# Kernel tuning notes

Measured on AMD Instinct MI355X. Metric: run time of the kernel, lower is better.

The kernel has to match this reference:

```python
import jax, jax.numpy as jnp
import numpy as np

HIDDEN = 128
SIGMA_D = 0.2
SIGMA_A = 15.0
ANGLE_K = 8
FACTOR_A = 180.0 / (SIGMA_A * np.pi)


def pairwise_sqdist(x, y):
    # x: (B,N,3), y: (B,M,3) -> (B,N,M) squared distances, clamped at 0
    sq = (jnp.sum(x * x, -1)[:, :, None]
          + jnp.sum(y * y, -1)[:, None, :]
          - 2.0 * jnp.einsum('bnd,bmd->bnm', x, y))
    return jnp.maximum(sq, 0.0)


def sinusoidal_embedding(indices, d_model):
    # indices: (...,) -> (..., d_model) with interleaved sin/cos (GeoTransformer style)
    div_term = jnp.exp(jnp.arange(0, d_model, 2, dtype=indices.dtype)
                       * (-np.log(10000.0) / d_model))
    omegas = indices[..., None] * div_term  # (..., d_model/2)
    emb = jnp.stack([jnp.sin(omegas), jnp.cos(omegas)], axis=-1)
    return emb.reshape(*indices.shape, d_model)


def setup_inputs() -> dict:
    key = jax.random.key(0)
    k1, k2, k3, k4, k5 = jax.random.split(key, 5)
    B, N, H = 1, 512, HIDDEN
    bound = 1.0 / np.sqrt(H)
    return {
        'points': jax.random.normal(k1, (B, N, 3), dtype=jnp.float32),
        'Wd': jax.random.uniform(k2, (H, H), jnp.float32, -bound, bound),
        'bd': jax.random.uniform(k3, (H,), jnp.float32, -bound, bound),
        'Wa': jax.random.uniform(k4, (H, H), jnp.float32, -bound, bound),
        'ba': jax.random.uniform(k5, (H,), jnp.float32, -bound, bound),
    }


def _embedding_indices(points):
    # points: (B,N,3) -> d_indices (B,N,N), a_indices (B,N,N,k)
    B, N, _ = points.shape
    sqdist = pairwise_sqdist(points, points)
    dist_map = jnp.sqrt(sqdist)
    d_indices = dist_map / SIGMA_D
    # knn (exclude self = nearest)
    _, knn_idx = jax.lax.top_k(-dist_map, ANGLE_K + 1)  # (B,N,k+1)
    knn_idx = knn_idx[:, :, 1:]                         # (B,N,k)
    # gather neighbor coords: (B,N,k,3)
    knn_points = jax.vmap(lambda pts, idx: pts[idx])(points, knn_idx)
    ref = knn_points - points[:, :, None, :]            # (B,N,k,3)
    anc = points[:, None, :, :] - points[:, :, None, :]  # (B,N,N,3)
    ref_e = ref[:, :, None, :, :]                        # (B,N,1,k,3)
    anc_e = anc[:, :, :, None, :]                        # (B,N,N,1,3)
    cross = jnp.cross(ref_e, anc_e)                      # (B,N,N,k,3)
    sin_v = jnp.linalg.norm(cross, axis=-1)
    cos_v = jnp.sum(ref_e * anc_e, axis=-1)
    angles = jnp.arctan2(sin_v, cos_v)
    a_indices = angles * FACTOR_A
    return d_indices, a_indices


def reference(points, Wd, bd, Wa, ba):
    d_indices, a_indices = _embedding_indices(points)
    d_emb = sinusoidal_embedding(d_indices, HIDDEN)      # (B,N,N,H)
    d_emb = jnp.einsum('bnmh,gh->bnmg', d_emb, Wd) + bd
    a_emb = sinusoidal_embedding(a_indices, HIDDEN)      # (B,N,N,k,H)
    a_emb = jnp.einsum('bnmkh,gh->bnmkg', a_emb, Wa) + ba
    a_emb = jnp.max(a_emb, axis=3)                       # reduction_a == 'max'
    return d_emb + a_emb
```

## Files before the change

### kernel.cpp

```cpp
#include <hip/hip_runtime.h>
#include <math.h>

#define N_PTS 512
#define HID 128
#define KNN 8
#define MT 16
#define NTHREADS 256
#define NROWS 144

typedef __attribute__((ext_vector_type(8))) short short8_t;
typedef __attribute__((ext_vector_type(4))) float f32x4_t;

__device__ float g_refv[N_PTS * KNN * 3];
__device__ unsigned short g_wfrag[2 * 8 * 4 * 64 * 8];

__device__ __forceinline__ unsigned short f2bf(float f) {
    const unsigned int u = __float_as_uint(f);
    return (unsigned short)((u + 0x7FFFu + ((u >> 16) & 1u)) >> 16);
}

__global__ void __launch_bounds__(64) prep_kernel(
    const float* __restrict__ points, const float* __restrict__ Wd,
    const float* __restrict__ Wa)
{
    __shared__ float spts[N_PTS * 3];
    const int lane = threadIdx.x;
    const int n = blockIdx.x;

    for (int i = lane; i < N_PTS * 3; i += 64) spts[i] = points[i];
    __syncthreads();

    {
        const int idx = n * 64 + lane;
        const int sel = idx >> 14;
        const int rem = idx & 16383;
        const int gg = rem >> 7, kk = rem & 127;
        const int gtile = gg >> 4, glo = gg & 15;
        const int ktile = kk >> 5, kmid = (kk >> 3) & 3, j = kk & 7;
        const int fl = kmid * 16 + glo;
        const int dst = ((((sel * 8 + gtile) * 4 + ktile) * 64) + fl) * 8 + j;
        const float v = sel ? Wa[gg * HID + kk] : Wd[gg * HID + kk];
        g_wfrag[dst] = f2bf(v);
    }

    const float px = spts[n * 3 + 0], py = spts[n * 3 + 1], pz = spts[n * 3 + 2];
    unsigned long long keys[8];
#pragma unroll
    for (int j = 0; j < 8; ++j) {
        const int m = lane * 8 + j;
        const float dx = spts[m * 3 + 0] - px;
        const float dy = spts[m * 3 + 1] - py;
        const float dz = spts[m * 3 + 2] - pz;
        const float sq = dx * dx + dy * dy + dz * dz;
        keys[j] = ((unsigned long long)__float_as_uint(sq) << 32) | (unsigned)m;
    }
    for (int r = 0; r < 9; ++r) {
        unsigned long long lmin = ~0ULL;
#pragma unroll
        for (int j = 0; j < 8; ++j) lmin = keys[j] < lmin ? keys[j] : lmin;
        for (int s = 1; s < 64; s <<= 1) {
            const unsigned long long o = __shfl_xor(lmin, s, 64);
            lmin = o < lmin ? o : lmin;
        }
        const int mwin = (int)(unsigned)lmin;
        if ((mwin >> 3) == lane) keys[mwin & 7] = ~0ULL;
        if (r > 0 && lane == 0) {
            const int k = r - 1;
            g_refv[(n * KNN + k) * 3 + 0] = __fsub_rn(spts[mwin * 3 + 0], px);
            g_refv[(n * KNN + k) * 3 + 1] = __fsub_rn(spts[mwin * 3 + 1], py);
            g_refv[(n * KNN + k) * 3 + 2] = __fsub_rn(spts[mwin * 3 + 2], pz);
        }
    }
}

__global__ void __launch_bounds__(NTHREADS, 3) main_kernel(
    const float* __restrict__ points, const float* __restrict__ bd,
    const float* __restrict__ ba, float* __restrict__ out)
{
    __shared__ __align__(16) unsigned short sA[NROWS * HID];
    __shared__ __align__(16) float sBaseS[4][36];
    __shared__ float sRef[KNN][3];
    __shared__ float sPm[MT][3];
    __shared__ float sPn[3];

    const int t = threadIdx.x;
    const int n = blockIdx.y;
    const int m0 = blockIdx.x * MT;

    const int r0 = t >> 6;
    const int i  = t & 63;
    const float dv2 = expf(-0.14391156831212787f * (float)i) * 0.15915494309189535f;

    if (t < 3) sPn[t] = points[n * 3 + t];
    if (t >= 64 && t < 64 + MT * 3) { int q = t - 64;  sPm[q / 3][q % 3] = points[m0 * 3 + q]; }
    if (t >= 128 && t < 128 + KNN * 3) { int q = t - 128; sRef[q / 3][q % 3] = g_refv[n * KNN * 3 + q]; }
    __syncthreads();

    if (t < MT) {
        const float qx = sPm[t][0], qy = sPm[t][1], qz = sPm[t][2];
        const float sn = __fadd_rn(__fadd_rn(__fmul_rn(sPn[0], sPn[0]), __fmul_rn(sPn[1], sPn[1])), __fmul_rn(sPn[2], sPn[2]));
        const float sm = __fadd_rn(__fadd_rn(__fmul_rn(qx, qx), __fmul_rn(qy, qy)), __fmul_rn(qz, qz));
        float dot = __fmul_rn(sPn[0], qx);
        dot = fmaf(sPn[1], qy, dot);
        dot = fmaf(sPn[2], qz, dot);
        float sq = __fsub_rn(__fadd_rn(sn, sm), __fadd_rn(dot, dot));
        sq = fmaxf(sq, 0.0f);
        sBaseS[t & 3][t >> 2] = __fdiv_rn(__fsqrt_rn(sq), 0.2f);
    }
    if (t < MT * KNN) {
        const int pair = t >> 3, k = t & 7;
        const float ax = sPm[pair][0] - sPn[0];
        const float ay = sPm[pair][1] - sPn[1];
        const float az = sPm[pair][2] - sPn[2];
        const float rx = sRef[k][0], ry = sRef[k][1], rz = sRef[k][2];
        const float cx = ry * az - rz * ay;
        const float cy = rz * ax - rx * az;
        const float cz = rx * ay - ry * ax;
        const float sv = sqrtf(cx * cx + cy * cy + cz * cz);
        const float cv = rx * ax + ry * ay + rz * az;
        float ang;
        if (sv == 0.0f) ang = 0.0f;
        else            ang = atan2f(sv, cv);
        sBaseS[pair & 3][4 + 4 * k + (pair >> 2)] = ang * 3.8197186342054885f;
    }
    __syncthreads();

    {
        float rbase[36];
#pragma unroll
        for (int q = 0; q < 9; ++q) {
            const float4 v = *(const float4*)&sBaseS[r0][q * 4];
            rbase[q * 4 + 0] = v.x; rbase[q * 4 + 1] = v.y;
            rbase[q * 4 + 2] = v.z; rbase[q * 4 + 3] = v.w;
        }
        const unsigned base0 = (unsigned)((i * 4) ^ (r0 << 4)) + (unsigned)r0 * 256;
        char* const wr0 = (char*)sA + base0;
        char* const wr1 = (char*)sA + (base0 ^ 64u);
#pragma unroll
        for (int it = 0; it < 36; ++it) {
            const float rev0 = rbase[it] * dv2;
            const float rev  = rev0 - floorf(rev0);
            const float s = __builtin_amdgcn_sinf(rev);
            const float c = __builtin_amdgcn_cosf(rev);
            const unsigned int pack = __builtin_amdgcn_perm(
                __float_as_uint(c), __float_as_uint(s), 0x07060302u);
            char* const wp = (it & 1) ? wr1 : wr0;
            *(unsigned int*)(wp + it * 1024) = pack;
        }
    }
    __syncthreads();

    const int wid  = r0;
    const int lane = i;
    const int rlo  = lane & 15;
    const int kseg = lane >> 4;

    const short8_t* wf = (const short8_t*)g_wfrag;
    short8_t wdb[2][4], wab[2][4];
#pragma unroll
    for (int gt = 0; gt < 2; ++gt) {
        const int gtile = wid * 2 + gt;
#pragma unroll
        for (int kt = 0; kt < 4; ++kt) {
            wdb[gt][kt] = wf[(gtile * 4 + kt) * 64 + lane];
            wab[gt][kt] = wf[((8 + gtile) * 4 + kt) * 64 + lane];
        }
    }

    const char* sAb = (const char*)sA;
    f32x4_t accd[2] = {{0.f,0.f,0.f,0.f}, {0.f,0.f,0.f,0.f}};
#pragma unroll
    for (int kt = 0; kt < 4; ++kt) {
        int byte = rlo * 256 + kt * 64 + kseg * 16;
        byte ^= (rlo & 7) << 4;
        const short8_t af = *(const short8_t*)(sAb + byte);
        accd[0] = __builtin_amdgcn_mfma_f32_16x16x32_bf16(af, wdb[0][kt], accd[0], 0, 0, 0);
        accd[1] = __builtin_amdgcn_mfma_f32_16x16x32_bf16(af, wdb[1][kt], accd[1], 0, 0, 0);
    }

    f32x4_t amax[2] = {{0.f,0.f,0.f,0.f}, {0.f,0.f,0.f,0.f}};
#pragma unroll
    for (int k = 0; k < KNN; ++k) {
        f32x4_t acc0 = {0.f,0.f,0.f,0.f};
        f32x4_t acc1 = {0.f,0.f,0.f,0.f};
        const int rowb = MT + k * 16 + rlo;
#pragma unroll
        for (int kt = 0; kt < 4; ++kt) {
            int byte = rowb * 256 + kt * 64 + kseg * 16;
            byte ^= (rowb & 7) << 4;
            const short8_t af = *(const short8_t*)(sAb + byte);
            acc0 = __builtin_amdgcn_mfma_f32_16x16x32_bf16(af, wab[0][kt], acc0, 0, 0, 0);
            acc1 = __builtin_amdgcn_mfma_f32_16x16x32_bf16(af, wab[1][kt], acc1, 0, 0, 0);
        }
        if (k == 0) { amax[0] = acc0; amax[1] = acc1; }
        else {
#pragma unroll
            for (int r = 0; r < 4; ++r) {
                amax[0][r] = fmaxf(amax[0][r], acc0[r]);
                amax[1][r] = fmaxf(amax[1][r], acc1[r]);
            }
        }
    }

#pragma unroll
    for (int gt = 0; gt < 2; ++gt) {
        const int g = (wid * 2 + gt) * 16 + rlo;
        const float bdv = bd[g];
        const float bav = ba[g];
#pragma unroll
        for (int r = 0; r < 4; ++r) {
            const int m = m0 + kseg * 4 + r;
            out[(n * N_PTS + m) * HID + g] = accd[gt][r] + bdv + amax[gt][r] + bav;
        }
    }
}

extern "C" void kernel_launch(void* const* d_in, const int* in_sizes, int n_in,
                              void* d_out, int out_size, void* d_ws, size_t ws_size,
                              hipStream_t stream) {
    (void)in_sizes; (void)n_in; (void)out_size; (void)d_ws; (void)ws_size;
    const float* points = (const float*)d_in[0];
    const float* Wd     = (const float*)d_in[1];
    const float* bd     = (const float*)d_in[2];
    const float* Wa     = (const float*)d_in[3];
    const float* ba     = (const float*)d_in[4];
    float* out = (float*)d_out;

    prep_kernel<<<N_PTS, 64, 0, stream>>>(points, Wd, Wa);

    dim3 grid(N_PTS / MT, N_PTS);
    main_kernel<<<grid, NTHREADS, 0, stream>>>(points, bd, ba, out);
}
```

Baseline: 112.6 us.

## Process four m-tiles per block with double-buffered sinusoid fill overlapping MFMA

Each block now handles four 16-point m-tiles. The weight fragments are loaded once per block, and the A-operand LDS buffer is double-buffered. The sin/cos embedding for the next tile is computed and written while MFMAs run on the current tile, interleaved inside one unrolled loop. This amortizes the weight loads and block setup, and it hides transcendental ALU work behind matrix ops. The cost is a smaller grid, double the LDS use, and occupancy lowered from 3 to 2 blocks in the launch bounds.

Result: faster. 108.1 us (median of 2 runs) (-4.0%).

```diff
diff --git a/kernel.cpp b/kernel.cpp
--- a/kernel.cpp
+++ b/kernel.cpp
@@ -5,6 +5,7 @@
 #define HID 128
 #define KNN 8
 #define MT 16
+#define NTILES 4
 #define NTHREADS 256
 #define NROWS 144
 
@@ -73,30 +74,44 @@
     }
 }
 
-__global__ void __launch_bounds__(NTHREADS, 3) main_kernel(
+__global__ void __launch_bounds__(NTHREADS, 2) main_kernel(
     const float* __restrict__ points, const float* __restrict__ bd,
     const float* __restrict__ ba, float* __restrict__ out)
 {
-    __shared__ __align__(16) unsigned short sA[NROWS * HID];
-    __shared__ __align__(16) float sBaseS[4][36];
+    __shared__ __align__(16) unsigned short sA[2][NROWS * HID];
+    __shared__ __align__(16) float sBaseS[NTILES][4][36];
     __shared__ float sRef[KNN][3];
-    __shared__ float sPm[MT][3];
+    __shared__ float sPm[MT * NTILES][3];
     __shared__ float sPn[3];
 
     const int t = threadIdx.x;
     const int n = blockIdx.y;
-    const int m0 = blockIdx.x * MT;
+    const int M0 = blockIdx.x * (MT * NTILES);
 
     const int r0 = t >> 6;
     const int i  = t & 63;
     const float dv2 = expf(-0.14391156831212787f * (float)i) * 0.15915494309189535f;
 
+    const int wid = r0, lane = i;
+    const short8_t* wf = (const short8_t*)g_wfrag;
+    short8_t wdb[2][4], wab[2][4];
+#pragma unroll
+    for (int gt = 0; gt < 2; ++gt) {
+        const int gtile = wid * 2 + gt;
+#pragma unroll
+        for (int kt = 0; kt < 4; ++kt) {
+            wdb[gt][kt] = wf[(gtile * 4 + kt) * 64 + lane];
+            wab[gt][kt] = wf[((8 + gtile) * 4 + kt) * 64 + lane];
+        }
+    }
+
     if (t < 3) sPn[t] = points[n * 3 + t];
-    if (t >= 64 && t < 64 + MT * 3) { int q = t - 64;  sPm[q / 3][q % 3] = points[m0 * 3 + q]; }
-    if (t >= 128 && t < 128 + KNN * 3) { int q = t - 128; sRef[q / 3][q % 3] = g_refv[n * KNN * 3 + q]; }
-    __syncthreads();
-
-    if (t < MT) {
+    if (t >= 8 && t < 8 + KNN * 3) { int q = t - 8; sRef[q / 3][q % 3] = g_refv[n * KNN * 3 + q]; }
+    if (t >= 64 && t < 64 + MT * NTILES * 3) { int q = t - 64; sPm[q / 3][q % 3] = points[M0 * 3 + q]; }
+    __syncthreads();
+
+    if (t < MT * NTILES) {
+        const int tt = t >> 4, pair = t & 15;
         const float qx = sPm[t][0], qy = sPm[t][1], qz = sPm[t][2];
         const float sn = __fadd_rn(__fadd_rn(__fmul_rn(sPn[0], sPn[0]), __fmul_rn(sPn[1], sPn[1])), __fmul_rn(sPn[2], sPn[2]));
         const float sm = __fadd_rn(__fadd_rn(__fmul_rn(qx, qx), __fmul_rn(qy, qy)), __fmul_rn(qz, qz));
@@ -105,13 +120,16 @@
         dot = fmaf(sPn[2], qz, dot);
         float sq = __fsub_rn(__fadd_rn(sn, sm), __fadd_rn(dot, dot));
         sq = fmaxf(sq, 0.0f);
-        sBaseS[t & 3][t >> 2] = __fdiv_rn(__fsqrt_rn(sq), 0.2f);
-    }
-    if (t < MT * KNN) {
-        const int pair = t >> 3, k = t & 7;
-        const float ax = sPm[pair][0] - sPn[0];
-        const float ay = sPm[pair][1] - sPn[1];
-        const float az = sPm[pair][2] - sPn[2];
+        sBaseS[tt][pair & 3][pair >> 2] = __fdiv_rn(__fsqrt_rn(sq), 0.2f);
+    }
+#pragma unroll
+    for (int q2 = 0; q2 < 2; ++q2) {
+        const int idx = q2 * 256 + t;
+        const int tt = idx >> 7, rem = idx & 127, pair = rem >> 3, k = rem & 7;
+        const int mp = tt * MT + pair;
+        const float ax = sPm[mp][0] - sPn[0];
+        const float ay = sPm[mp][1] - sPn[1];
+        const float az = sPm[mp][2] - sPn[2];
         const float rx = sRef[k][0], ry = sRef[k][1], rz = sRef[k][2];
         const float cx = ry * az - rz * ay;
         const float cy = rz * ax - rx * az;
@@ -121,21 +139,24 @@
         float ang;
         if (sv == 0.0f) ang = 0.0f;
         else            ang = atan2f(sv, cv);
-        sBaseS[pair & 3][4 + 4 * k + (pair >> 2)] = ang * 3.8197186342054885f;
-    }
-    __syncthreads();
+        sBaseS[tt][pair & 3][4 + 4 * k + (pair >> 2)] = ang * 3.8197186342054885f;
+    }
+    __syncthreads();
+
+    const unsigned base0 = (unsigned)((i * 4) ^ (r0 << 4)) + (unsigned)r0 * 256;
+    const int rlo  = lane & 15;
+    const int kseg = lane >> 4;
 
     {
         float rbase[36];
 #pragma unroll
         for (int q = 0; q < 9; ++q) {
-            const float4 v = *(const float4*)&sBaseS[r0][q * 4];
+            const float4 v = *(const float4*)&sBaseS[0][r0][q * 4];
             rbase[q * 4 + 0] = v.x; rbase[q * 4 + 1] = v.y;
             rbase[q * 4 + 2] = v.z; rbase[q * 4 + 3] = v.w;
         }
-        const unsigned base0 = (unsigned)((i * 4) ^ (r0 << 4)) + (unsigned)r0 * 256;
-        char* const wr0 = (char*)sA + base0;
-        char* const wr1 = (char*)sA + (base0 ^ 64u);
+        char* const wr0 = (char*)sA[0] + base0;
+        char* const wr1 = (char*)sA[0] + (base0 ^ 64u);
 #pragma unroll
         for (int it = 0; it < 36; ++it) {
             const float rev0 = rbase[it] * dv2;
@@ -150,68 +171,81 @@
     }
     __syncthreads();
 
-    const int wid  = r0;
-    const int lane = i;
-    const int rlo  = lane & 15;
-    const int kseg = lane >> 4;
-
-    const short8_t* wf = (const short8_t*)g_wfrag;
-    short8_t wdb[2][4], wab[2][4];
-#pragma unroll
-    for (int gt = 0; gt < 2; ++gt) {
-        const int gtile = wid * 2 + gt;
-#pragma unroll
-        for (int kt = 0; kt < 4; ++kt) {
-            wdb[gt][kt] = wf[(gtile * 4 + kt) * 64 + lane];
-            wab[gt][kt] = wf[((8 + gtile) * 4 + kt) * 64 + lane];
-        }
-    }
-
-    const char* sAb = (const char*)sA;
-    f32x4_t accd[2] = {{0.f,0.f,0.f,0.f}, {0.f,0.f,0.f,0.f}};
-#pragma unroll
-    for (int kt = 0; kt < 4; ++kt) {
-        int byte = rlo * 256 + kt * 64 + kseg * 16;
-        byte ^= (rlo & 7) << 4;
-        const short8_t af = *(const short8_t*)(sAb + byte);
-        accd[0] = __builtin_amdgcn_mfma_f32_16x16x32_bf16(af, wdb[0][kt], accd[0], 0, 0, 0);
-        accd[1] = __builtin_amdgcn_mfma_f32_16x16x32_bf16(af, wdb[1][kt], accd[1], 0, 0, 0);
-    }
-
-    f32x4_t amax[2] = {{0.f,0.f,0.f,0.f}, {0.f,0.f,0.f,0.f}};
-#pragma unroll
-    for (int k = 0; k < KNN; ++k) {
-        f32x4_t acc0 = {0.f,0.f,0.f,0.f};
-        f32x4_t acc1 = {0.f,0.f,0.f,0.f};
-        const int rowb = MT + k * 16 + rlo;
-#pragma unroll
-        for (int kt = 0; kt < 4; ++kt) {
-            int byte = rowb * 256 + kt * 64 + kseg * 16;
-            byte ^= (rowb & 7) << 4;
-            const short8_t af = *(const short8_t*)(sAb + byte);
-            acc0 = __builtin_amdgcn_mfma_f32_16x16x32_bf16(af, wab[0][kt], acc0, 0, 0, 0);
-            acc1 = __builtin_amdgcn_mfma_f32_16x16x32_bf16(af, wab[1][kt], acc1, 0, 0, 0);
-        }
-        if (k == 0) { amax[0] = acc0; amax[1] = acc1; }
-        else {
+    const f32x4_t vz = {0.f, 0.f, 0.f, 0.f};
+#pragma unroll
+    for (int tt = 0; tt < NTILES; ++tt) {
+        const char* sAb = (const char*)sA[tt & 1];
+        const bool dofill = (tt < NTILES - 1);
+
+        float rbase[36];
+        char* wr0 = (char*)sA[(tt + 1) & 1] + base0;
+        char* wr1 = (char*)sA[(tt + 1) & 1] + (base0 ^ 64u);
+        if (dofill) {
+#pragma unroll
+            for (int q = 0; q < 9; ++q) {
+                const float4 v = *(const float4*)&sBaseS[tt + 1][r0][q * 4];
+                rbase[q * 4 + 0] = v.x; rbase[q * 4 + 1] = v.y;
+                rbase[q * 4 + 2] = v.z; rbase[q * 4 + 3] = v.w;
+            }
+        }
+
+        f32x4_t accd[2] = {vz, vz};
+        f32x4_t amax[2] = {vz, vz};
+        f32x4_t acc0 = vz, acc1 = vz;
+
+#pragma unroll
+        for (int it = 0; it < 36; ++it) {
+            if (dofill) {
+                const float rev0 = rbase[it] * dv2;
+                const float rev  = rev0 - floorf(rev0);
+                const float s = __builtin_amdgcn_sinf(rev);
+                const float c = __builtin_amdgcn_cosf(rev);
+                const unsigned int pack = __builtin_amdgcn_perm(
+                    __float_as_uint(c), __float_as_uint(s), 0x07060302u);
+                char* const wp = (it & 1) ? wr1 : wr0;
+                *(unsigned int*)(wp + it * 1024) = pack;
+            }
+            if (it < 4) {
+                const int kt = it;
+                int byte = rlo * 256 + kt * 64 + kseg * 16;
+                byte ^= (rlo & 7) << 4;
+                const short8_t af = *(const short8_t*)(sAb + byte);
+                accd[0] = __builtin_amdgcn_mfma_f32_16x16x32_bf16(af, wdb[0][kt], accd[0], 0, 0, 0);
+                accd[1] = __builtin_amdgcn_mfma_f32_16x16x32_bf16(af, wdb[1][kt], accd[1], 0, 0, 0);
+            } else {
+                const int q = it - 4, k = q >> 2, kt = q & 3;
+                const int rowb = MT + k * 16 + rlo;
+                int byte = rowb * 256 + kt * 64 + kseg * 16;
+                byte ^= (rowb & 7) << 4;
+                const short8_t af = *(const short8_t*)(sAb + byte);
+                acc0 = __builtin_amdgcn_mfma_f32_16x16x32_bf16(af, wab[0][kt], acc0, 0, 0, 0);
+                acc1 = __builtin_amdgcn_mfma_f32_16x16x32_bf16(af, wab[1][kt], acc1, 0, 0, 0);
+                if (kt == 3) {
+                    if (k == 0) { amax[0] = acc0; amax[1] = acc1; }
+                    else {
+#pragma unroll
+                        for (int r = 0; r < 4; ++r) {
+                            amax[0][r] = fmaxf(amax[0][r], acc0[r]);
+                            amax[1][r] = fmaxf(amax[1][r], acc1[r]);
+                        }
+                    }
+                    acc0 = vz; acc1 = vz;
+                }
+            }
+        }
+
+#pragma unroll
+        for (int gt = 0; gt < 2; ++gt) {
+            const int g = (wid * 2 + gt) * 16 + rlo;
+            const float bdv = bd[g];
+            const float bav = ba[g];
 #pragma unroll
             for (int r = 0; r < 4; ++r) {
-                amax[0][r] = fmaxf(amax[0][r], acc0[r]);
-                amax[1][r] = fmaxf(amax[1][r], acc1[r]);
-            }
-        }
-    }
-
-#pragma unroll
-    for (int gt = 0; gt < 2; ++gt) {
-        const int g = (wid * 2 + gt) * 16 + rlo;
-        const float bdv = bd[g];
-        const float bav = ba[g];
-#pragma unroll
-        for (int r = 0; r < 4; ++r) {
-            const int m = m0 + kseg * 4 + r;
-            out[(n * N_PTS + m) * HID + g] = accd[gt][r] + bdv + amax[gt][r] + bav;
-        }
+                const int m = M0 + tt * MT + kseg * 4 + r;
+                out[(n * N_PTS + m) * HID + g] = accd[gt][r] + bdv + amax[gt][r] + bav;
+            }
+        }
+        __syncthreads();
     }
 }
 
@@ -228,6 +262,6 @@
 
     prep_kernel<<<N_PTS, 64, 0, stream>>>(points, Wd, Wa);
 
-    dim3 grid(N_PTS / MT, N_PTS);
+    dim3 grid(N_PTS / (MT * NTILES), N_PTS);
     main_kernel<<<grid, NTHREADS, 0, stream>>>(points, bd, ba, out);
 }
```

## Compute angle embedding GEMM with 32x32x16 MFMA and in-register k-max

Applied to the files above, without the earlier changes.

Replaces the per-neighbor 16x16x32 MFMA loop for the angle projection with 32x32x16 bf16 MFMAs. Rows are arranged so that the 8 neighbors of each point land in one accumulator tile, which lets the max over neighbors be taken inside registers plus a single cross-half shuffle. A new Wa fragment layout is prepared in the prep kernel. The per-wave angle max results are then staged through a new 8 KB shared buffer and read back by the distance-output threads. This adds a barrier and more LDS per block, which may lower occupancy.

Result: slower. 146.7 us (+30.3%).

```diff
diff --git a/kernel.cpp b/kernel.cpp
--- a/kernel.cpp
+++ b/kernel.cpp
@@ -10,9 +10,11 @@
 
 typedef __attribute__((ext_vector_type(8))) short short8_t;
 typedef __attribute__((ext_vector_type(4))) float f32x4_t;
+typedef __attribute__((ext_vector_type(16))) float f32x16_t;
 
 __device__ float g_refv[N_PTS * KNN * 3];
 __device__ unsigned short g_wfrag[2 * 8 * 4 * 64 * 8];
+__device__ unsigned short g_wfrag32[4 * 8 * 64 * 8];
 
 __device__ __forceinline__ unsigned short f2bf(float f) {
     const unsigned int u = __float_as_uint(f);
@@ -42,6 +44,15 @@
         const float v = sel ? Wa[gg * HID + kk] : Wd[gg * HID + kk];
         g_wfrag[dst] = f2bf(v);
     }
+    if (lane < 32) {
+        const int idx = n * 32 + lane;
+        const int gg = idx >> 7, kk = idx & 127;
+        const int ggroup = gg >> 5, c = gg & 31;
+        const int kchunk = kk >> 4, hi2 = (kk >> 3) & 1, j = kk & 7;
+        const int fl = hi2 * 32 + c;
+        const int dst = ((ggroup * 8 + kchunk) * 64 + fl) * 8 + j;
+        g_wfrag32[dst] = f2bf(Wa[gg * HID + kk]);
+    }
 
     const float px = spts[n * 3 + 0], py = spts[n * 3 + 1], pz = spts[n * 3 + 2];
     unsigned long long keys[8];
@@ -78,6 +89,7 @@
     const float* __restrict__ ba, float* __restrict__ out)
 {
     __shared__ __align__(16) unsigned short sA[NROWS * HID];
+    __shared__ __align__(16) float sOut[MT * HID];
     __shared__ __align__(16) float sBaseS[4][36];
     __shared__ float sRef[KNN][3];
     __shared__ float sPm[MT][3];
@@ -150,24 +162,54 @@
     }
     __syncthreads();
 
-    const int wid  = r0;
-    const int lane = i;
+    const int wid = r0, lane = i;
+    const char* sAb = (const char*)sA;
+
+    const int c31 = lane & 31;
+    const int hi  = lane >> 5;
+    const int arow = MT + (c31 >> 2) * 16 + wid * 4 + (c31 & 3);
+    const int aswz = (arow & 7) << 4;
+    short8_t afr[8];
+#pragma unroll
+    for (int kc = 0; kc < 8; ++kc) {
+        const int byte = (arow * 256 + kc * 32 + hi * 16) ^ aswz;
+        afr[kc] = *(const short8_t*)(sAb + byte);
+    }
+    const short8_t* wf32 = (const short8_t*)g_wfrag32;
+#pragma unroll
+    for (int half = 0; half < 2; ++half) {
+        const int g0 = half * 2, g1 = half * 2 + 1;
+        f32x16_t a0 = {0.f,0.f,0.f,0.f,0.f,0.f,0.f,0.f,0.f,0.f,0.f,0.f,0.f,0.f,0.f,0.f};
+        f32x16_t a1 = {0.f,0.f,0.f,0.f,0.f,0.f,0.f,0.f,0.f,0.f,0.f,0.f,0.f,0.f,0.f,0.f};
+#pragma unroll
+        for (int kc = 0; kc < 8; ++kc) {
+            a0 = __builtin_amdgcn_mfma_f32_32x32x16_bf16(afr[kc], wf32[(g0 * 8 + kc) * 64 + lane], a0, 0, 0, 0);
+            a1 = __builtin_amdgcn_mfma_f32_32x32x16_bf16(afr[kc], wf32[(g1 * 8 + kc) * 64 + lane], a1, 0, 0, 0);
+        }
+#pragma unroll
+        for (int m = 0; m < 4; ++m) {
+            float v0 = fmaxf(fmaxf(a0[m], a0[m + 4]), fmaxf(a0[m + 8], a0[m + 12]));
+            float v1 = fmaxf(fmaxf(a1[m], a1[m + 4]), fmaxf(a1[m + 8], a1[m + 12]));
+            v0 = fmaxf(v0, __shfl_xor(v0, 32, 64));
+            v1 = fmaxf(v1, __shfl_xor(v1, 32, 64));
+            if (hi == 0) {
+                sOut[(wid * 4 + m) * HID + g0 * 32 + c31] = v0;
+                sOut[(wid * 4 + m) * HID + g1 * 32 + c31] = v1;
+            }
+        }
+    }
+
     const int rlo  = lane & 15;
     const int kseg = lane >> 4;
-
     const short8_t* wf = (const short8_t*)g_wfrag;
-    short8_t wdb[2][4], wab[2][4];
+    short8_t wdb[2][4];
 #pragma unroll
     for (int gt = 0; gt < 2; ++gt) {
         const int gtile = wid * 2 + gt;
 #pragma unroll
-        for (int kt = 0; kt < 4; ++kt) {
+        for (int kt = 0; kt < 4; ++kt)
             wdb[gt][kt] = wf[(gtile * 4 + kt) * 64 + lane];
-            wab[gt][kt] = wf[((8 + gtile) * 4 + kt) * 64 + lane];
-        }
-    }
-
-    const char* sAb = (const char*)sA;
+    }
     f32x4_t accd[2] = {{0.f,0.f,0.f,0.f}, {0.f,0.f,0.f,0.f}};
 #pragma unroll
     for (int kt = 0; kt < 4; ++kt) {
@@ -178,29 +220,7 @@
         accd[1] = __builtin_amdgcn_mfma_f32_16x16x32_bf16(af, wdb[1][kt], accd[1], 0, 0, 0);
     }
 
-    f32x4_t amax[2] = {{0.f,0.f,0.f,0.f}, {0.f,0.f,0.f,0.f}};
-#pragma unroll
-    for (int k = 0; k < KNN; ++k) {
-        f32x4_t acc0 = {0.f,0.f,0.f,0.f};
-        f32x4_t acc1 = {0.f,0.f,0.f,0.f};
-        const int rowb = MT + k * 16 + rlo;
-#pragma unroll
-        for (int kt = 0; kt < 4; ++kt) {
-            int byte = rowb * 256 + kt * 64 + kseg * 16;
-            byte ^= (rowb & 7) << 4;
-            const short8_t af = *(const short8_t*)(sAb + byte);
-            acc0 = __builtin_amdgcn_mfma_f32_16x16x32_bf16(af, wab[0][kt], acc0, 0, 0, 0);
-            acc1 = __builtin_amdgcn_mfma_f32_16x16x32_bf16(af, wab[1][kt], acc1, 0, 0, 0);
-        }
-        if (k == 0) { amax[0] = acc0; amax[1] = acc1; }
-        else {
-#pragma unroll
-            for (int r = 0; r < 4; ++r) {
-                amax[0][r] = fmaxf(amax[0][r], acc0[r]);
-                amax[1][r] = fmaxf(amax[1][r], acc1[r]);
-            }
-        }
-    }
+    __syncthreads();
 
 #pragma unroll
     for (int gt = 0; gt < 2; ++gt) {
@@ -209,8 +229,8 @@
         const float bav = ba[g];
 #pragma unroll
         for (int r = 0; r < 4; ++r) {
-            const int m = m0 + kseg * 4 + r;
-            out[(n * N_PTS + m) * HID + g] = accd[gt][r] + bdv + amax[gt][r] + bav;
+            const int m = kseg * 4 + r;
+            out[(n * N_PTS + (m0 + m)) * HID + g] = accd[gt][r] + bdv + sOut[m * HID + g] + bav;
         }
     }
 }
```

## Split MFMA work across waves by neighbor set and output-column half

Applied to the files above, without the earlier changes.

Before, each of the four waves computed two 16-column output tiles over all eight neighbors. Now waves are arranged as two column halves (four tiles each) by two neighbor halves. The partial max is combined through a new shared buffer after an extra barrier, and only the neighbor-set-0 waves compute the distance GEMM and write the output. Each A fragment loaded from shared memory now feeds four MFMAs instead of two, which cuts LDS reads. In exchange, per-wave register use rises (16 weight fragments plus 4 accumulators), work is uneven between waves, and the added shared memory and sync may hurt occupancy.

Measured after the change: 125.1 us. 1.11x slower.

```diff
diff --git a/kernel.cpp b/kernel.cpp
--- a/kernel.cpp
+++ b/kernel.cpp
@@ -78,6 +78,7 @@
     const float* __restrict__ ba, float* __restrict__ out)
 {
     __shared__ __align__(16) unsigned short sA[NROWS * HID];
+    __shared__ __align__(16) float sOutP[8][MT][17];
     __shared__ __align__(16) float sBaseS[4][36];
     __shared__ float sRef[KNN][3];
     __shared__ float sPm[MT][3];
@@ -152,65 +153,92 @@
 
     const int wid  = r0;
     const int lane = i;
+    const int gset = wid & 1;
+    const int kset = wid >> 1;
     const int rlo  = lane & 15;
     const int kseg = lane >> 4;
 
     const short8_t* wf = (const short8_t*)g_wfrag;
-    short8_t wdb[2][4], wab[2][4];
-#pragma unroll
-    for (int gt = 0; gt < 2; ++gt) {
-        const int gtile = wid * 2 + gt;
+    const char* sAb = (const char*)sA;
+    const f32x4_t vz = {0.f, 0.f, 0.f, 0.f};
+
+    f32x4_t accd[4] = {vz, vz, vz, vz};
+    if (kset == 0) {
+        short8_t wdb[4][4];
+#pragma unroll
+        for (int gt = 0; gt < 4; ++gt) {
+            const int gtile = gset * 4 + gt;
+#pragma unroll
+            for (int kt = 0; kt < 4; ++kt)
+                wdb[gt][kt] = wf[(gtile * 4 + kt) * 64 + lane];
+        }
 #pragma unroll
         for (int kt = 0; kt < 4; ++kt) {
-            wdb[gt][kt] = wf[(gtile * 4 + kt) * 64 + lane];
+            int byte = rlo * 256 + kt * 64 + kseg * 16;
+            byte ^= (rlo & 7) << 4;
+            const short8_t af = *(const short8_t*)(sAb + byte);
+#pragma unroll
+            for (int gt = 0; gt < 4; ++gt)
+                accd[gt] = __builtin_amdgcn_mfma_f32_16x16x32_bf16(af, wdb[gt][kt], accd[gt], 0, 0, 0);
+        }
+    }
+
+    short8_t wab[4][4];
+#pragma unroll
+    for (int gt = 0; gt < 4; ++gt) {
+        const int gtile = gset * 4 + gt;
+#pragma unroll
+        for (int kt = 0; kt < 4; ++kt)
             wab[gt][kt] = wf[((8 + gtile) * 4 + kt) * 64 + lane];
-        }
-    }
-
-    const char* sAb = (const char*)sA;
-    f32x4_t accd[2] = {{0.f,0.f,0.f,0.f}, {0.f,0.f,0.f,0.f}};
-#pragma unroll
-    for (int kt = 0; kt < 4; ++kt) {
-        int byte = rlo * 256 + kt * 64 + kseg * 16;
-        byte ^= (rlo & 7) << 4;
-        const short8_t af = *(const short8_t*)(sAb + byte);
-        accd[0] = __builtin_amdgcn_mfma_f32_16x16x32_bf16(af, wdb[0][kt], accd[0], 0, 0, 0);
-        accd[1] = __builtin_amdgcn_mfma_f32_16x16x32_bf16(af, wdb[1][kt], accd[1], 0, 0, 0);
-    }
-
-    f32x4_t amax[2] = {{0.f,0.f,0.f,0.f}, {0.f,0.f,0.f,0.f}};
-#pragma unroll
-    for (int k = 0; k < KNN; ++k) {
-        f32x4_t acc0 = {0.f,0.f,0.f,0.f};
-        f32x4_t acc1 = {0.f,0.f,0.f,0.f};
-        const int rowb = MT + k * 16 + rlo;
+    }
+    f32x4_t amax[4] = {vz, vz, vz, vz};
+#pragma unroll
+    for (int kl = 0; kl < 4; ++kl) {
+        const int kk = kset * 4 + kl;
+        const int rowb = MT + kk * 16 + rlo;
+        f32x4_t acc[4] = {vz, vz, vz, vz};
 #pragma unroll
         for (int kt = 0; kt < 4; ++kt) {
             int byte = rowb * 256 + kt * 64 + kseg * 16;
             byte ^= (rowb & 7) << 4;
             const short8_t af = *(const short8_t*)(sAb + byte);
-            acc0 = __builtin_amdgcn_mfma_f32_16x16x32_bf16(af, wab[0][kt], acc0, 0, 0, 0);
-            acc1 = __builtin_amdgcn_mfma_f32_16x16x32_bf16(af, wab[1][kt], acc1, 0, 0, 0);
-        }
-        if (k == 0) { amax[0] = acc0; amax[1] = acc1; }
-        else {
+#pragma unroll
+            for (int gt = 0; gt < 4; ++gt)
+                acc[gt] = __builtin_amdgcn_mfma_f32_16x16x32_bf16(af, wab[gt][kt], acc[gt], 0, 0, 0);
+        }
+        if (kl == 0) {
+#pragma unroll
+            for (int gt = 0; gt < 4; ++gt) amax[gt] = acc[gt];
+        } else {
+#pragma unroll
+            for (int gt = 0; gt < 4; ++gt)
+#pragma unroll
+                for (int r = 0; r < 4; ++r)
+                    amax[gt][r] = fmaxf(amax[gt][r], acc[gt][r]);
+        }
+    }
+
+    if (kset == 1) {
+#pragma unroll
+        for (int gt = 0; gt < 4; ++gt)
+#pragma unroll
+            for (int r = 0; r < 4; ++r)
+                sOutP[gset * 4 + gt][kseg * 4 + r][rlo] = amax[gt][r];
+    }
+    __syncthreads();
+
+    if (kset == 0) {
+#pragma unroll
+        for (int gt = 0; gt < 4; ++gt) {
+            const int g = (gset * 4 + gt) * 16 + rlo;
+            const float bdv = bd[g];
+            const float bav = ba[g];
 #pragma unroll
             for (int r = 0; r < 4; ++r) {
-                amax[0][r] = fmaxf(amax[0][r], acc0[r]);
-                amax[1][r] = fmaxf(amax[1][r], acc1[r]);
+                const int m = kseg * 4 + r;
+                const float ax = fmaxf(amax[gt][r], sOutP[gset * 4 + gt][m][rlo]);
+                out[(n * N_PTS + (m0 + m)) * HID + g] = accd[gt][r] + bdv + ax + bav;
             }
-        }
-    }
-
-#pragma unroll
-    for (int gt = 0; gt < 2; ++gt) {
-        const int g = (wid * 2 + gt) * 16 + rlo;
-        const float bdv = bd[g];
-        const float bav = ba[g];
-#pragma unroll
-        for (int r = 0; r < 4; ++r) {
-            const int m = m0 + kseg * 4 + r;
-            out[(n * N_PTS + m) * HID + g] = accd[gt][r] + bdv + amax[gt][r] + bav;
         }
     }
 }
```
